# Kernel optimization log

Hardware: AMD Instinct MI355X
Metric: run time of the kernel (lower is better)

Reference implementation:

```python
import jax, jax.numpy as jnp
import numpy as np

B, S, D, UNITS = 8, 2048, 512, 512

def setup_inputs() -> dict:
    key = jax.random.key(0)
    k1, k2, k3, k4 = jax.random.split(key, 4)
    scale = 1.0 / np.sqrt(D)
    return {
        "x": jax.random.normal(k1, (B, S, D), dtype=jnp.float32),
        "Wq": jax.random.normal(k2, (D, UNITS), dtype=jnp.float32) * scale,
        "Wk": jax.random.normal(k3, (D, UNITS), dtype=jnp.float32) * scale,
        "Wv": jax.random.normal(k4, (D, UNITS), dtype=jnp.float32) * scale,
    }

def reference(x, Wq, Wk, Wv):
    # Q, K, V: [B, S, units]
    Q = jnp.einsum('bsd,du->bsu', x, Wq)
    Km = jnp.einsum('bsd,du->bsu', x, Wk)
    V = jnp.einsum('bsd,du->bsu', x, Wv)
    d_k = jnp.asarray(Wq.shape[-1], dtype=x.dtype)
    # scores: [B, S, S]
    scores = jnp.einsum('bqu,bku->bqk', Q, Km) / jnp.sqrt(d_k)
    attn = jax.nn.softmax(scores, axis=-1)
    return jnp.einsum('bqk,bku->bqu', attn, V)
```

## Files before the change

### kernel.cpp

```cpp
#include <hip/hip_runtime.h>

typedef __attribute__((ext_vector_type(8))) __bf16 bf16x8;
typedef __attribute__((ext_vector_type(4))) float f32x4;
typedef unsigned short u16;
typedef unsigned int u32;

#define VMCNT(n) asm volatile("s_waitcnt vmcnt(" #n ")" ::: "memory")

__device__ __forceinline__ u16 f2bf(float f) {
  union { float f; u32 u; } v; v.f = f;
  u32 r = v.u + 0x7FFFu + ((v.u >> 16) & 1u);
  return (u16)(r >> 16);
}
__device__ __forceinline__ float fexp2(float x) {
  float r; asm("v_exp_f32 %0, %1" : "=v"(r) : "v"(x)); return r;
}

__global__ __launch_bounds__(256) void cast_x_kernel(const float* __restrict__ x,
                                                     u16* __restrict__ xb, int n4) {
  int i = blockIdx.x * 256 + threadIdx.x;
  if (i >= n4) return;
  float4 v = reinterpret_cast<const float4*>(x)[i];
  ushort4 o;
  o.x = f2bf(v.x); o.y = f2bf(v.y); o.z = f2bf(v.z); o.w = f2bf(v.w);
  reinterpret_cast<ushort4*>(xb)[i] = o;
}

__global__ __launch_bounds__(1024) void transpose_w_kernel(const float* __restrict__ Wq,
                                                           const float* __restrict__ Wk,
                                                           const float* __restrict__ Wv,
                                                           u16* __restrict__ Wt) {
  const float* src = blockIdx.z == 0 ? Wq : (blockIdx.z == 1 ? Wk : Wv);
  u16* dst = Wt + (size_t)blockIdx.z * 512 * 512;
  __shared__ float tile[32][33];
  int u0 = blockIdx.x * 32, d0 = blockIdx.y * 32;
  tile[threadIdx.y][threadIdx.x] = src[(d0 + threadIdx.y) * 512 + u0 + threadIdx.x];
  __syncthreads();
  dst[(u0 + threadIdx.y) * 512 + d0 + threadIdx.x] = f2bf(tile[threadIdx.x][threadIdx.y]);
}

__global__ __launch_bounds__(256) void qkv_kernel(const u16* __restrict__ Xb,
                                                  const u16* __restrict__ Wt3,
                                                  u16* __restrict__ Q, u16* __restrict__ K,
                                                  u16* __restrict__ Vt) {
  __shared__ u16 As[3][128 * 32], Bs[3][128 * 32];
  const int bm = blockIdx.y * 128;
  const int bn = blockIdx.x * 128;
  const int z = blockIdx.z;
  const u16* A = Xb + (size_t)bm * 512;
  const u16* Bt = Wt3 + (size_t)z * 512 * 512 + (size_t)bn * 512;

  const int t = threadIdx.x;
  const int lane = t & 63;
  const int w = t >> 6;
  const int wr = w >> 1, wc = w & 1;
  const int la = lane & 15;
  const int q = lane >> 4;
  f32x4 acc[4][4] = {};

  auto stage = [&](int buf, int kt) {
    const int k0 = kt * 32;
#pragma unroll
    for (int it = 0; it < 2; ++it) {
      int c = it * 256 + t, row = c >> 2;
      int col = ((c & 3) ^ ((row >> 1) & 3)) << 3;
      __builtin_amdgcn_global_load_lds(
          (const __attribute__((address_space(1))) void*)(A + (size_t)row * 512 + k0 + col),
          (__attribute__((address_space(3))) void*)(&As[buf][c * 8]), 16, 0, 0);
    }
#pragma unroll
    for (int it = 0; it < 2; ++it) {
      int c = it * 256 + t, row = c >> 2;
      int col = ((c & 3) ^ ((row >> 1) & 3)) << 3;
      __builtin_amdgcn_global_load_lds(
          (const __attribute__((address_space(1))) void*)(Bt + (size_t)row * 512 + k0 + col),
          (__attribute__((address_space(3))) void*)(&Bs[buf][c * 8]), 16, 0, 0);
    }
  };

  auto body = [&](int buf) {
    bf16x8 a[4], b[4];
#pragma unroll
    for (int i = 0; i < 4; ++i) {
      int row = wr * 64 + i * 16 + la;
      a[i] = *reinterpret_cast<const bf16x8*>(&As[buf][row * 32 + ((q ^ ((row >> 1) & 3)) << 3)]);
    }
#pragma unroll
    for (int j = 0; j < 4; ++j) {
      int row = wc * 64 + j * 16 + la;
      b[j] = *reinterpret_cast<const bf16x8*>(&Bs[buf][row * 32 + ((q ^ ((row >> 1) & 3)) << 3)]);
    }
    __builtin_amdgcn_s_setprio(1);
#pragma unroll
    for (int i = 0; i < 4; ++i)
#pragma unroll
      for (int j = 0; j < 4; ++j)
        acc[i][j] = __builtin_amdgcn_mfma_f32_16x16x32_bf16(a[i], b[j], acc[i][j], 0, 0, 0);
    __builtin_amdgcn_s_setprio(0);
  };

  stage(0, 0); stage(1, 1);
  int cb = 0, sb = 2;
  for (int kt = 0; kt < 14; ++kt) {
    VMCNT(4);
    __builtin_amdgcn_s_barrier();
    stage(sb, kt + 2);
    body(cb);
    cb = (cb == 2) ? 0 : cb + 1;
    sb = (sb == 2) ? 0 : sb + 1;
  }
  VMCNT(4); __builtin_amdgcn_s_barrier(); body(2);
  VMCNT(0); __builtin_amdgcn_s_barrier(); body(0);

  const int r0 = q * 4, cn = lane & 15;
  if (z < 2) {
    u16* out = (z == 0) ? Q : K;
#pragma unroll
    for (int i = 0; i < 4; ++i)
#pragma unroll
      for (int j = 0; j < 4; ++j)
#pragma unroll
        for (int r = 0; r < 4; ++r) {
          int m = bm + 64 * wr + 16 * i + r0 + r;
          int n = bn + 64 * wc + 16 * j + cn;
          out[(size_t)m * 512 + n] = f2bf(acc[i][j][r]);
        }
  } else {
#pragma unroll
    for (int i = 0; i < 4; ++i)
#pragma unroll
      for (int j = 0; j < 4; ++j)
#pragma unroll
        for (int r = 0; r < 4; ++r) {
          int m = bm + 64 * wr + 16 * i + r0 + r;
          int u = bn + 64 * wc + 16 * j + cn;
          int b = m >> 11, s = m & 2047;
          Vt[((size_t)b * 512 + u) * 2048 + s] = f2bf(acc[i][j][r]);
        }
  }
}

__global__ __launch_bounds__(512) void scores8_kernel(const u16* __restrict__ Q,
                                                      const u16* __restrict__ K,
                                                      u16* __restrict__ S) {
  __shared__ u16 ring[4][2][256 * 32];
  const int bb = blockIdx.x;
  const int bm = blockIdx.y * 256;
  const int bn = blockIdx.z * 256;
  const u16* Aq = Q + (size_t)(bb * 2048 + bm) * 512;
  const u16* Bk = K + (size_t)(bb * 2048 + bn) * 512;

  const int t = threadIdx.x;
  const int lane = t & 63;
  const int wid = t >> 6;
  const int wm = wid >> 2, wn = wid & 3;
  const int la = lane & 15;
  const int q = lane >> 4;

  f32x4 acc[8][4] = {};

  auto stage = [&](int kt) {
    const int r = kt & 3;
    const int koff = kt * 32;
#pragma unroll
    for (int half = 0; half < 2; ++half) {
      int c = half * 512 + t;
      int row = c >> 2;
      int col = ((c & 3) ^ ((row >> 1) & 3)) << 3;
      __builtin_amdgcn_global_load_lds(
          (const __attribute__((address_space(1))) void*)(Aq + (size_t)row * 512 + koff + col),
          (__attribute__((address_space(3))) void*)(&ring[r][0][c * 8]), 16, 0, 0);
      __builtin_amdgcn_global_load_lds(
          (const __attribute__((address_space(1))) void*)(Bk + (size_t)row * 512 + koff + col),
          (__attribute__((address_space(3))) void*)(&ring[r][1][c * 8]), 16, 0, 0);
    }
  };

  auto body = [&](int kt) {
    const int r = kt & 3;
    const u16* At = ring[r][0];
    const u16* Bt = ring[r][1];
    bf16x8 bfr[4], afr[8];
#pragma unroll
    for (int j = 0; j < 4; ++j) {
      int row = wn * 64 + j * 16 + la;
      bfr[j] = *reinterpret_cast<const bf16x8*>(Bt + row * 32 + ((q ^ ((row >> 1) & 3)) << 3));
    }
#pragma unroll
    for (int i = 0; i < 8; ++i) {
      int row = wm * 128 + i * 16 + la;
      afr[i] = *reinterpret_cast<const bf16x8*>(At + row * 32 + ((q ^ ((row >> 1) & 3)) << 3));
    }
    __builtin_amdgcn_s_setprio(1);
#pragma unroll
    for (int i = 0; i < 8; ++i)
#pragma unroll
      for (int j = 0; j < 4; ++j)
        acc[i][j] = __builtin_amdgcn_mfma_f32_16x16x32_bf16(afr[i], bfr[j], acc[i][j], 0, 0, 0);
    __builtin_amdgcn_s_setprio(0);
  };

  stage(0); stage(1); stage(2);
  for (int kt = 0; kt < 13; ++kt) {
    VMCNT(8);
    __builtin_amdgcn_s_barrier();
    stage(kt + 3);
    body(kt);
  }
  VMCNT(8); __builtin_amdgcn_s_barrier(); body(13);
  VMCNT(4); __builtin_amdgcn_s_barrier(); body(14);
  VMCNT(0); __builtin_amdgcn_s_barrier(); body(15);

  u16* C = S + (size_t)bb * 2048 * 2048;
  const float scale = 0.06375872127f;
  const int r0h = q * 4;
#pragma unroll
  for (int i = 0; i < 8; ++i)
#pragma unroll
    for (int j = 0; j < 4; ++j)
#pragma unroll
      for (int r = 0; r < 4; ++r) {
        int m = bm + wm * 128 + i * 16 + r0h + r;
        int n = bn + wn * 64 + j * 16 + la;
        C[(size_t)m * 2048 + n] = f2bf(fexp2(acc[i][j][r] * scale));
      }
}

__global__ __launch_bounds__(256) void pv_kernel(const u16* __restrict__ S,
                                                 const u16* __restrict__ Vt,
                                                 float* __restrict__ out) {
  __shared__ u16 As[3][128 * 32], Bs[3][128 * 32];
  __shared__ float larr[128];
  const int id = blockIdx.x;
  const int b = id & 7;
  const int local = id >> 3;
  const int bn = (local & 3) * 128;
  const int bm = (local >> 2) * 128;

  const u16* A = S + (size_t)(b * 2048 + bm) * 2048;
  const u16* Bt = Vt + ((size_t)b * 512 + bn) * 2048;

  const int t = threadIdx.x;
  const int lane = t & 63;
  const int w = t >> 6;
  const int wr = w >> 1, wc = w & 1;
  const int la = lane & 15;
  const int q = lane >> 4;
  f32x4 acc[4][4] = {};
  float lacc[4] = {0.f, 0.f, 0.f, 0.f};

  auto stage = [&](int buf, int kt) {
    const int k0 = kt * 32;
#pragma unroll
    for (int it = 0; it < 2; ++it) {
      int c = it * 256 + t, row = c >> 2;
      int col = ((c & 3) ^ ((row >> 1) & 3)) << 3;
      __builtin_amdgcn_global_load_lds(
          (const __attribute__((address_space(1))) void*)(A + (size_t)row * 2048 + k0 + col),
          (__attribute__((address_space(3))) void*)(&As[buf][c * 8]), 16, 0, 0);
    }
#pragma unroll
    for (int it = 0; it < 2; ++it) {
      int c = it * 256 + t, row = c >> 2;
      int col = ((c & 3) ^ ((row >> 1) & 3)) << 3;
      __builtin_amdgcn_global_load_lds(
          (const __attribute__((address_space(1))) void*)(Bt + (size_t)row * 2048 + k0 + col),
          (__attribute__((address_space(3))) void*)(&Bs[buf][c * 8]), 16, 0, 0);
    }
  };

  auto body = [&](int buf) {
    bf16x8 a[4], bb[4];
#pragma unroll
    for (int i = 0; i < 4; ++i) {
      int row = wr * 64 + i * 16 + la;
      a[i] = *reinterpret_cast<const bf16x8*>(&As[buf][row * 32 + ((q ^ ((row >> 1) & 3)) << 3)]);
    }
    if (wc == 0) {
#pragma unroll
      for (int i = 0; i < 4; ++i) {
        float ls = 0.f;
#pragma unroll
        for (int e = 0; e < 8; ++e) ls += (float)a[i][e];
        lacc[i] += ls;
      }
    }
#pragma unroll
    for (int j = 0; j < 4; ++j) {
      int row = wc * 64 + j * 16 + la;
      bb[j] = *reinterpret_cast<const bf16x8*>(&Bs[buf][row * 32 + ((q ^ ((row >> 1) & 3)) << 3)]);
    }
    __builtin_amdgcn_s_setprio(1);
#pragma unroll
    for (int i = 0; i < 4; ++i)
#pragma unroll
      for (int j = 0; j < 4; ++j)
        acc[i][j] = __builtin_amdgcn_mfma_f32_16x16x32_bf16(a[i], bb[j], acc[i][j], 0, 0, 0);
    __builtin_amdgcn_s_setprio(0);
  };

  stage(0, 0); stage(1, 1);
  int cb = 0, sb = 2;
  for (int kt = 0; kt < 62; ++kt) {
    VMCNT(4);
    __builtin_amdgcn_s_barrier();
    stage(sb, kt + 2);
    body(cb);
    cb = (cb == 2) ? 0 : cb + 1;
    sb = (sb == 2) ? 0 : sb + 1;
  }
  VMCNT(4); __builtin_amdgcn_s_barrier(); body(2);
  VMCNT(0); __builtin_amdgcn_s_barrier(); body(0);

  float l[4];
#pragma unroll
  for (int i = 0; i < 4; ++i) {
    l[i] = lacc[i];
    l[i] += __shfl_xor(l[i], 16);
    l[i] += __shfl_xor(l[i], 32);
  }
  if (wc == 0 && q == 0) {
#pragma unroll
    for (int i = 0; i < 4; ++i) larr[wr * 64 + i * 16 + la] = l[i];
  }
  __syncthreads();

  float* C = out + ((size_t)b * 2048 + bm) * 512;
  const int r0 = q * 4, cn = lane & 15;
  float inv[4][4];
#pragma unroll
  for (int i = 0; i < 4; ++i)
#pragma unroll
    for (int r = 0; r < 4; ++r)
      inv[i][r] = 1.0f / larr[wr * 64 + i * 16 + r0 + r];
#pragma unroll
  for (int i = 0; i < 4; ++i)
#pragma unroll
    for (int j = 0; j < 4; ++j)
#pragma unroll
      for (int r = 0; r < 4; ++r) {
        int m = 64 * wr + 16 * i + r0 + r;
        int n = bn + 64 * wc + 16 * j + cn;
        C[(size_t)m * 512 + n] = acc[i][j][r] * inv[i][r];
      }
}

extern "C" void kernel_launch(void* const* d_in, const int* in_sizes, int n_in,
                              void* d_out, int out_size, void* d_ws, size_t ws_size,
                              hipStream_t stream) {
  const float* x  = (const float*)d_in[0];
  const float* Wq = (const float*)d_in[1];
  const float* Wk = (const float*)d_in[2];
  const float* Wv = (const float*)d_in[3];
  float* out = (float*)d_out;

  char* p = (char*)d_ws;
  u16* Xb = (u16*)p;            p += (size_t)16384 * 512 * 2;
  u16* Wt = (u16*)p;            p += (size_t)3 * 512 * 512 * 2;
  u16* Q  = (u16*)p;            p += (size_t)16384 * 512 * 2;
  u16* K  = (u16*)p;            p += (size_t)16384 * 512 * 2;
  u16* Vt = (u16*)p;            p += (size_t)16384 * 512 * 2;
  u16* S  = (u16*)p;

  cast_x_kernel<<<dim3(8192), dim3(256), 0, stream>>>(x, Xb, 16384 * 512 / 4);
  transpose_w_kernel<<<dim3(16, 16, 3), dim3(32, 32), 0, stream>>>(Wq, Wk, Wv, Wt);
  qkv_kernel<<<dim3(4, 128, 3), dim3(256), 0, stream>>>(Xb, Wt, Q, K, Vt);
  scores8_kernel<<<dim3(8, 8, 8), dim3(512), 0, stream>>>(Q, K, S);
  pv_kernel<<<dim3(512), dim3(256), 0, stream>>>(S, Vt, out);
}
```

Measured before the change: 152.9 us.

## Load PV operands directly from global into registers, drop LDS staging

```diff
diff --git a/kernel.cpp b/kernel.cpp
--- a/kernel.cpp
+++ b/kernel.cpp
@@ -226,10 +226,9 @@
       }
 }
 
-__global__ __launch_bounds__(256) void pv_kernel(const u16* __restrict__ S,
-                                                 const u16* __restrict__ Vt,
-                                                 float* __restrict__ out) {
-  __shared__ u16 As[3][128 * 32], Bs[3][128 * 32];
+__global__ __launch_bounds__(256, 2) void pv_kernel(const u16* __restrict__ S,
+                                                    const u16* __restrict__ Vt,
+                                                    float* __restrict__ out) {
   __shared__ float larr[128];
   const int id = blockIdx.x;
   const int b = id & 7;
@@ -237,45 +236,31 @@
   const int bn = (local & 3) * 128;
   const int bm = (local >> 2) * 128;
 
-  const u16* A = S + (size_t)(b * 2048 + bm) * 2048;
-  const u16* Bt = Vt + ((size_t)b * 512 + bn) * 2048;
-
   const int t = threadIdx.x;
   const int lane = t & 63;
   const int w = t >> 6;
   const int wr = w >> 1, wc = w & 1;
   const int la = lane & 15;
   const int q = lane >> 4;
+
+  const u16* Abase = S + (size_t)(b * 2048 + bm + wr * 64 + la) * 2048 + q * 8;
+  const u16* Bbase = Vt + (size_t)(b * 512 + bn + wc * 64 + la) * 2048 + q * 8;
+
   f32x4 acc[4][4] = {};
   float lacc[4] = {0.f, 0.f, 0.f, 0.f};
 
-  auto stage = [&](int buf, int kt) {
-    const int k0 = kt * 32;
-#pragma unroll
-    for (int it = 0; it < 2; ++it) {
-      int c = it * 256 + t, row = c >> 2;
-      int col = ((c & 3) ^ ((row >> 1) & 3)) << 3;
-      __builtin_amdgcn_global_load_lds(
-          (const __attribute__((address_space(1))) void*)(A + (size_t)row * 2048 + k0 + col),
-          (__attribute__((address_space(3))) void*)(&As[buf][c * 8]), 16, 0, 0);
-    }
-#pragma unroll
-    for (int it = 0; it < 2; ++it) {
-      int c = it * 256 + t, row = c >> 2;
-      int col = ((c & 3) ^ ((row >> 1) & 3)) << 3;
-      __builtin_amdgcn_global_load_lds(
-          (const __attribute__((address_space(1))) void*)(Bt + (size_t)row * 2048 + k0 + col),
-          (__attribute__((address_space(3))) void*)(&Bs[buf][c * 8]), 16, 0, 0);
-    }
-  };
-
-  auto body = [&](int buf) {
-    bf16x8 a[4], bb[4];
-#pragma unroll
-    for (int i = 0; i < 4; ++i) {
-      int row = wr * 64 + i * 16 + la;
-      a[i] = *reinterpret_cast<const bf16x8*>(&As[buf][row * 32 + ((q ^ ((row >> 1) & 3)) << 3)]);
-    }
+  bf16x8 af[4][4], bf[4][4];
+
+  auto lda = [&](bf16x8 (&a)[4], bf16x8 (&bb)[4], int kt) {
+#pragma unroll
+    for (int i = 0; i < 4; ++i)
+      a[i] = *reinterpret_cast<const bf16x8*>(Abase + (size_t)i * 16 * 2048 + kt * 32);
+#pragma unroll
+    for (int j = 0; j < 4; ++j)
+      bb[j] = *reinterpret_cast<const bf16x8*>(Bbase + (size_t)j * 16 * 2048 + kt * 32);
+  };
+
+  auto body = [&](bf16x8 (&a)[4], bf16x8 (&bb)[4]) {
     if (wc == 0) {
 #pragma unroll
       for (int i = 0; i < 4; ++i) {
@@ -285,11 +270,6 @@
         lacc[i] += ls;
       }
     }
-#pragma unroll
-    for (int j = 0; j < 4; ++j) {
-      int row = wc * 64 + j * 16 + la;
-      bb[j] = *reinterpret_cast<const bf16x8*>(&Bs[buf][row * 32 + ((q ^ ((row >> 1) & 3)) << 3)]);
-    }
     __builtin_amdgcn_s_setprio(1);
 #pragma unroll
     for (int i = 0; i < 4; ++i)
@@ -299,18 +279,21 @@
     __builtin_amdgcn_s_setprio(0);
   };
 
-  stage(0, 0); stage(1, 1);
-  int cb = 0, sb = 2;
-  for (int kt = 0; kt < 62; ++kt) {
-    VMCNT(4);
-    __builtin_amdgcn_s_barrier();
-    stage(sb, kt + 2);
-    body(cb);
-    cb = (cb == 2) ? 0 : cb + 1;
-    sb = (sb == 2) ? 0 : sb + 1;
-  }
-  VMCNT(4); __builtin_amdgcn_s_barrier(); body(2);
-  VMCNT(0); __builtin_amdgcn_s_barrier(); body(0);
+  lda(af[0], bf[0], 0);
+  lda(af[1], bf[1], 1);
+  lda(af[2], bf[2], 2);
+  lda(af[3], bf[3], 3);
+  for (int it = 0; it < 15; ++it) {
+    const int kt = it * 4;
+    body(af[0], bf[0]); lda(af[0], bf[0], kt + 4);
+    body(af[1], bf[1]); lda(af[1], bf[1], kt + 5);
+    body(af[2], bf[2]); lda(af[2], bf[2], kt + 6);
+    body(af[3], bf[3]); lda(af[3], bf[3], kt + 7);
+  }
+  body(af[0], bf[0]);
+  body(af[1], bf[1]);
+  body(af[2], bf[2]);
+  body(af[3], bf[3]);
 
   float l[4];
 #pragma unroll
```

After: 216.8 us. 1.42x slower.
